# Kernel tuning notes

Measured on AMD Instinct MI355X. Metric: run time of the kernel, lower is better.

The kernel has to match this reference:

```python
import jax, jax.numpy as jnp
import numpy as np

N, E, IN_DIM, HID = 100000, 1600000, 128, 256
AA_DIM, POS_DIM, MAX_POS = 64, 32, 512


def setup_inputs() -> dict:
    key = jax.random.key(0)
    ks = jax.random.split(key, 16)
    x = jax.random.normal(ks[0], (N, IN_DIM), dtype=jnp.float32)
    edge_index = jax.random.randint(ks[1], (2, E), 0, N, dtype=jnp.int64)
    edge_weight = jax.random.uniform(ks[2], (E,), dtype=jnp.float32)
    mut_mask = jnp.zeros((N,), dtype=jnp.float32).at[123].set(1.0)  # one-hot mutation site
    wt_idx = jax.random.randint(ks[3], (1,), 0, 20, dtype=jnp.int64)
    mut_idx = jax.random.randint(ks[4], (1,), 0, 20, dtype=jnp.int64)
    def glorot(k, shape):
        fan = shape[0] + shape[1]
        return jax.random.uniform(k, shape, jnp.float32, -1.0, 1.0) * np.sqrt(6.0 / fan)
    W1 = glorot(ks[5], (IN_DIM, HID)); b1 = jnp.zeros((HID,), jnp.float32)
    W2 = glorot(ks[6], (HID, HID));    b2 = jnp.zeros((HID,), jnp.float32)
    aa_emb = jax.random.normal(ks[7], (20, AA_DIM), dtype=jnp.float32)
    pos_emb = jax.random.normal(ks[8], (MAX_POS, POS_DIM), dtype=jnp.float32)
    FEAT = HID + AA_DIM * 3 + POS_DIM  # 480
    Wh1 = glorot(ks[9], (FEAT, 512));  bh1 = jnp.zeros((512,), jnp.float32)
    Wh2 = glorot(ks[10], (512, 128));  bh2 = jnp.zeros((128,), jnp.float32)
    Wh3 = glorot(ks[11], (128, 1));    bh3 = jnp.zeros((1,), jnp.float32)
    return dict(x=x, edge_index=edge_index, edge_weight=edge_weight, mut_mask=mut_mask,
                wt_idx=wt_idx, mut_idx=mut_idx, W1=W1, b1=b1, W2=W2, b2=b2,
                aa_emb=aa_emb, pos_emb=pos_emb, Wh1=Wh1, bh1=bh1, Wh2=Wh2, bh2=bh2,
                Wh3=Wh3, bh3=bh3)


def _gcn_conv(x, W, b, row, col, ew, n):
    # PyG GCNConv: h = x W; out[col] += norm * h[row]; norm = d^-1/2[row]*ew*d^-1/2[col]
    deg = jax.ops.segment_sum(ew, col, num_segments=n)
    dinv = jnp.where(deg > 0, jax.lax.rsqrt(jnp.maximum(deg, 1e-12)), 0.0)
    norm = dinv[row] * ew * dinv[col]
    h = x @ W
    out = jax.ops.segment_sum(h[row] * norm[:, None], col, num_segments=n)
    return out + b


def reference(x, edge_index, edge_weight, mut_mask, wt_idx, mut_idx,
              W1, b1, W2, b2, aa_emb, pos_emb, Wh1, bh1, Wh2, bh2, Wh3, bh3):
    n = x.shape[0]
    # add self loops with weight 1 (GCNConv default, fill_value=1.0)
    loop = jnp.arange(n, dtype=edge_index.dtype)
    row = jnp.concatenate([edge_index[0], loop])
    col = jnp.concatenate([edge_index[1], loop])
    ew = jnp.concatenate([edge_weight, jnp.ones((n,), edge_weight.dtype)])
    # encode (dropout is identity in eval mode)
    h = jax.nn.relu(_gcn_conv(x, W1, b1, row, col, ew, n))
    h = jax.nn.relu(_gcn_conv(h, W2, b2, row, col, ew, n))
    # masked sum -> [1, HID]
    z = (h * mut_mask[:, None]).sum(axis=0, keepdims=True)
    wt = aa_emb[wt_idx.reshape(-1)]
    mut = aa_emb[mut_idx.reshape(-1)]
    delta = mut - wt
    pos = jnp.clip(jnp.argmax(mut_mask), 0, pos_emb.shape[0] - 1).reshape(1)
    pe = pos_emb[pos]
    feat = jnp.concatenate([z, wt, mut, delta, pe], axis=1)  # [1, 480]
    f = jax.nn.relu(feat @ Wh1 + bh1)
    f = jax.nn.relu(f @ Wh2 + bh2)
    out = f @ Wh3 + bh3  # [1, 1]
    return out[0, 0]
```

## Files before the change

### kernel.cpp

```cpp
#include <hip/hip_runtime.h>


#define SCAP   512
#define L1CAP  512
#define L2CAP  16384
#define HID    256
#define INDIM  128

struct WsPtrs {
  int* cnt;
  float* deg;
  int* slot;
  int* s1;
  int* l1r; float* l1w;
  int* l2r; int* l2s; float* l2w;
  float* h1; float* h2;
  int* wscol;
};

__global__ void kinit(WsPtrs w, const int* eiraw, const float* mask, int N, int E) {
  int g = blockIdx.x * blockDim.x + threadIdx.x;
  int gs = gridDim.x * blockDim.x;
  for (int j = g; j < N; j += gs) {
    w.slot[j] = -1;
    float m = mask[j];
    if (m > 0.f) w.cnt[4] = j;
  }
  for (int j = g; j < SCAP * HID; j += gs) w.h1[j] = 0.f;
  if (g < HID) w.h2[g] = 0.f;
  if (g < 3)   w.cnt[g] = 0;
  if (g == 3) {
    int is64 = 1;
    long step = E / 20; if (step < 1) step = 1;
    for (int j = 1; j <= 16; ++j) {
      long idx = (long)j * step; if (idx >= E) break;
      if (eiraw[2 * idx + 1] != 0) { is64 = 0; break; }
    }
    w.cnt[3] = is64;
  }
}

__device__ __forceinline__ void reg_s1(WsPtrs& w, int r) {
  int old = atomicCAS(&w.slot[r], -1, -2);
  if (old == -1) {
    w.deg[r] = 1.0f;
    int idx = atomicAdd(&w.cnt[1], 1);
    if (idx < SCAP) { w.s1[idx] = r; w.slot[r] = idx; }
    else            { w.slot[r] = -3; }
  }
}

__global__ void kpassA(WsPtrs w, const int* eiraw, const float* ew, int E) {
  const int tgt = w.cnt[4];
  const bool is64 = w.cnt[3] != 0;
  const long long* ell = (const long long*)eiraw;
  int g = blockIdx.x * blockDim.x + threadIdx.x;
  int gs = gridDim.x * blockDim.x;
  for (long e = g; e < E; e += gs) {
    int c = is64 ? (int)ell[(long)E + e] : eiraw[(long)E + e];
    w.wscol[e] = c;
    if (c == tgt) {
      int r = is64 ? (int)ell[e] : eiraw[e];
      int i1 = atomicAdd(&w.cnt[0], 1);
      if (i1 < L1CAP) { w.l1r[i1] = r; w.l1w[i1] = ew[e]; }
      reg_s1(w, r);
    }
  }
  if (g == 0) {
    int i1 = atomicAdd(&w.cnt[0], 1);
    if (i1 < L1CAP) { w.l1r[i1] = tgt; w.l1w[i1] = 1.0f; }
    reg_s1(w, tgt);
  }
}

__global__ void kpassB(WsPtrs w, const int* eiraw, const float* ew, int E) {
  const bool is64 = w.cnt[3] != 0;
  const long long* ell = (const long long*)eiraw;
  int g = blockIdx.x * blockDim.x + threadIdx.x;
  int gs = gridDim.x * blockDim.x;
  int ns = w.cnt[1]; if (ns > SCAP) ns = SCAP;
  for (int j = g; j < ns; j += gs) {
    int idx = atomicAdd(&w.cnt[2], 1);
    if (idx < L2CAP) { w.l2r[idx] = w.s1[j]; w.l2s[idx] = j; w.l2w[idx] = 1.0f; }
  }
  const int4* c4 = (const int4*)w.wscol;
  int nv = E >> 2;
  for (int j = g; j < nv; j += gs) {
    int4 v = c4[j];
    #pragma unroll
    for (int t = 0; t < 4; ++t) {
      int c = (t == 0) ? v.x : (t == 1) ? v.y : (t == 2) ? v.z : v.w;
      int s = w.slot[c];
      if (s >= 0) {
        long e = 4L * j + t;
        int r = is64 ? (int)ell[e] : eiraw[e];
        int idx = atomicAdd(&w.cnt[2], 1);
        if (idx < L2CAP) { w.l2r[idx] = r; w.l2s[idx] = s; w.l2w[idx] = ew[e]; }
        int old = atomicCAS(&w.slot[r], -1, -3);
        if (old == -1) w.deg[r] = 1.0f;
      }
    }
  }
  for (long e = 4L * nv + g; e < E; e += gs) {
    int c = w.wscol[e];
    int s = w.slot[c];
    if (s >= 0) {
      int r = is64 ? (int)ell[e] : eiraw[e];
      int idx = atomicAdd(&w.cnt[2], 1);
      if (idx < L2CAP) { w.l2r[idx] = r; w.l2s[idx] = s; w.l2w[idx] = ew[e]; }
      int old = atomicCAS(&w.slot[r], -1, -3);
      if (old == -1) w.deg[r] = 1.0f;
    }
  }
}

__global__ void kpassC(WsPtrs w, const float* ew, int E) {
  int g = blockIdx.x * blockDim.x + threadIdx.x;
  int gs = gridDim.x * blockDim.x;
  const int4* c4 = (const int4*)w.wscol;
  int nv = E >> 2;
  for (int j = g; j < nv; j += gs) {
    int4 v = c4[j];
    #pragma unroll
    for (int t = 0; t < 4; ++t) {
      int c = (t == 0) ? v.x : (t == 1) ? v.y : (t == 2) ? v.z : v.w;
      if (w.slot[c] != -1) atomicAdd(&w.deg[c], ew[4L * j + t]);
    }
  }
  for (long e = 4L * nv + g; e < E; e += gs) {
    int c = w.wscol[e];
    if (w.slot[c] != -1) atomicAdd(&w.deg[c], ew[e]);
  }
}

__global__ void kh1(WsPtrs w, const float* x, const float* W1) {
  __shared__ float xs[INDIM];
  int n = w.cnt[2]; if (n > L2CAP) n = L2CAP;
  int tid = threadIdx.x;
  for (int b = blockIdx.x; b < n; b += gridDim.x) {
    int r = w.l2r[b], s = w.l2s[b];
    float wt = w.l2w[b];
    int c = w.s1[s];
    float norm = rsqrtf(w.deg[r]) * wt * rsqrtf(w.deg[c]);
    if (tid < INDIM) xs[tid] = x[(long)r * INDIM + tid];
    __syncthreads();
    float acc = 0.f;
    #pragma unroll 8
    for (int k = 0; k < INDIM; ++k) acc += xs[k] * W1[k * HID + tid];
    atomicAdd(&w.h1[s * HID + tid], norm * acc);
    __syncthreads();
  }
}

__global__ void kh2(WsPtrs w, const float* W2, const float* b1) {
  __shared__ float hs[HID];
  int n = w.cnt[0]; if (n > L1CAP) n = L1CAP;
  int tid = threadIdx.x;
  int tgt = w.cnt[4];
  float dti = rsqrtf(w.deg[tgt]);
  for (int b = blockIdx.x; b < n; b += gridDim.x) {
    int v = w.l1r[b]; float wt = w.l1w[b];
    int s = w.slot[v];
    hs[tid] = (s >= 0) ? fmaxf(w.h1[s * HID + tid] + b1[tid], 0.f) : 0.f;
    __syncthreads();
    float norm = rsqrtf(w.deg[v]) * wt * dti;
    float acc = 0.f;
    #pragma unroll 8
    for (int k = 0; k < HID; ++k) acc += hs[k] * W2[k * HID + tid];
    atomicAdd(&w.h2[tid], norm * acc);
    __syncthreads();
  }
}

__global__ void __launch_bounds__(1024) khead(
    WsPtrs w, const float* b2, const float* mask,
    const int* wtI_, const int* mutI_,
    const float* aa, const float* pemb,
    const float* Wh1, const float* bh1,
    const float* Wh2, const float* bh2,
    const float* Wh3, const float* bh3,
    float* out) {
  __shared__ float feat[480];
  __shared__ float f1[512];
  __shared__ float pp[1024];
  __shared__ float f2[128];
  int t = threadIdx.x;
  int tgt = w.cnt[4];
  if (t < HID) feat[t] = fmaxf(w.h2[t] + b2[t], 0.f) * mask[tgt];
  int wtI = wtI_[0], mutI = mutI_[0];
  if (t < 64) {
    float a = aa[wtI * 64 + t];
    float b = aa[mutI * 64 + t];
    feat[256 + t] = a; feat[320 + t] = b; feat[384 + t] = b - a;
  }
  int pos = tgt; if (pos > 511) pos = 511; if (pos < 0) pos = 0;
  if (t < 32) feat[448 + t] = pemb[pos * 32 + t];
  __syncthreads();
  {
    int o = t & 511, half = t >> 9;
    int k0 = half * 240, k1 = k0 + 240;
    float v = 0.f;
    for (int k = k0; k < k1; ++k) v += feat[k] * Wh1[k * 512 + o];
    pp[t] = v;
  }
  __syncthreads();
  if (t < 512) f1[t] = fmaxf(pp[t] + pp[t + 512] + bh1[t], 0.f);
  __syncthreads();
  {
    int o = t & 127, part = t >> 7;
    int k0 = part * 64, k1 = k0 + 64;
    float v = 0.f;
    for (int k = k0; k < k1; ++k) v += f1[k] * Wh2[k * 128 + o];
    pp[t] = v;
  }
  __syncthreads();
  if (t < 128) {
    float v = bh2[t];
    #pragma unroll
    for (int j = 0; j < 8; ++j) v += pp[j * 128 + t];
    f2[t] = fmaxf(v, 0.f) * Wh3[t];
  }
  __syncthreads();
  if (t == 0) {
    float s = bh3[0];
    for (int k = 0; k < 128; ++k) s += f2[k];
    out[0] = s;
  }
}

extern "C" void kernel_launch(void* const* d_in, const int* in_sizes, int n_in,
                              void* d_out, int out_size, void* d_ws, size_t ws_size,
                              hipStream_t stream) {
  const float* x    = (const float*)d_in[0];
  const int*   ei   = (const int*)d_in[1];
  const float* ew   = (const float*)d_in[2];
  const float* mask = (const float*)d_in[3];
  const int*   wtI  = (const int*)d_in[4];
  const int*   mutI = (const int*)d_in[5];
  const float* W1   = (const float*)d_in[6];
  const float* b1   = (const float*)d_in[7];
  const float* W2   = (const float*)d_in[8];
  const float* b2   = (const float*)d_in[9];
  const float* aa   = (const float*)d_in[10];
  const float* pemb = (const float*)d_in[11];
  const float* Wh1  = (const float*)d_in[12];
  const float* bh1  = (const float*)d_in[13];
  const float* Wh2  = (const float*)d_in[14];
  const float* bh2  = (const float*)d_in[15];
  const float* Wh3  = (const float*)d_in[16];
  const float* bh3  = (const float*)d_in[17];
  float* out = (float*)d_out;
  const int N = in_sizes[3];
  const int E = in_sizes[2];

  char* q = (char*)d_ws;
  auto take = [&](size_t bytes) -> char* {
    char* r = q; q += (bytes + 255) & ~(size_t)255; return r;
  };
  WsPtrs w;
  w.cnt   = (int*)take(64);
  w.deg   = (float*)take((size_t)N * 4);
  w.slot  = (int*)take((size_t)N * 4);
  w.s1    = (int*)take(SCAP * 4);
  w.l1r   = (int*)take(L1CAP * 4);
  w.l1w   = (float*)take(L1CAP * 4);
  w.l2r   = (int*)take(L2CAP * 4);
  w.l2s   = (int*)take(L2CAP * 4);
  w.l2w   = (float*)take(L2CAP * 4);
  w.h1    = (float*)take((size_t)SCAP * HID * 4);
  w.h2    = (float*)take(HID * 4);
  w.wscol = (int*)take((size_t)E * 4);

  kinit  <<<512, 256, 0, stream>>>(w, ei, mask, N, E);
  kpassA <<<2048, 256, 0, stream>>>(w, ei, ew, E);
  kpassB <<<1024, 256, 0, stream>>>(w, ei, ew, E);
  kpassC <<<1024, 256, 0, stream>>>(w, ew, E);
  kh1    <<<512, 256, 0, stream>>>(w, x, W1);
  kh2    <<<64, 256, 0, stream>>>(w, W2, b1);
  khead  <<<1, 1024, 0, stream>>>(w, b2, mask, wtI, mutI, aa, pemb,
                                  Wh1, bh1, Wh2, bh2, Wh3, bh3, out);
}
```

Baseline: 183.4 us.

## Aggregate inputs before W1 and fuse layer/head kernels with last-block reduction

Layer-1 aggregation now sums the normalized neighbour input rows for each 1-hop node first and applies W1 once per node, instead of doing one matmul per 2-hop edge. The slot table, the materialized column array and the separate degree pass are removed. Degrees are computed for all nodes inside the first edge pass. kh1, kh2 and khead are merged into one 64-block kernel that uses a last-block-done atomic counter to run W2 and the MLP head. The trade-offs are a degree atomic for every edge, a linear scan over the 1-hop list in shared memory for every edge in pass B, and serial per-neighbour row accumulation with single-block tail work.

```diff
diff --git a/kernel.cpp b/kernel.cpp
--- a/kernel.cpp
+++ b/kernel.cpp
@@ -4,49 +4,39 @@
 #define SCAP   512
 #define L1CAP  512
 #define L2CAP  16384
+#define MCAP   2048
 #define HID    256
 #define INDIM  128
+#define G4     64
 
 struct WsPtrs {
   int* cnt;
   float* deg;
-  int* slot;
   int* s1;
   int* l1r; float* l1w;
   int* l2r; int* l2s; float* l2w;
-  float* h1; float* h2;
-  int* wscol;
+  float* h2;
 };
 
 __global__ void kinit(WsPtrs w, const int* eiraw, const float* mask, int N, int E) {
   int g = blockIdx.x * blockDim.x + threadIdx.x;
   int gs = gridDim.x * blockDim.x;
   for (int j = g; j < N; j += gs) {
-    w.slot[j] = -1;
-    float m = mask[j];
-    if (m > 0.f) w.cnt[4] = j;
-  }
-  for (int j = g; j < SCAP * HID; j += gs) w.h1[j] = 0.f;
+    w.deg[j] = 1.0f;
+    if (mask[j] > 0.f) w.cnt[4] = j;
+  }
   if (g < HID) w.h2[g] = 0.f;
-  if (g < 3)   w.cnt[g] = 0;
+  if (g < 3) w.cnt[g] = 0;
+  if (g == 5) w.cnt[5] = 0;
   if (g == 3) {
-    int is64 = 1;
+    int bad = 0;
     long step = E / 20; if (step < 1) step = 1;
+    #pragma unroll
     for (int j = 1; j <= 16; ++j) {
-      long idx = (long)j * step; if (idx >= E) break;
-      if (eiraw[2 * idx + 1] != 0) { is64 = 0; break; }
-    }
-    w.cnt[3] = is64;
-  }
-}
-
-__device__ __forceinline__ void reg_s1(WsPtrs& w, int r) {
-  int old = atomicCAS(&w.slot[r], -1, -2);
-  if (old == -1) {
-    w.deg[r] = 1.0f;
-    int idx = atomicAdd(&w.cnt[1], 1);
-    if (idx < SCAP) { w.s1[idx] = r; w.slot[r] = idx; }
-    else            { w.slot[r] = -3; }
+      long idx = (long)j * step;
+      if (idx < E) bad |= (eiraw[2 * idx + 1] != 0);
+    }
+    w.cnt[3] = bad ? 0 : 1;
   }
 }
 
@@ -58,173 +48,172 @@
   int gs = gridDim.x * blockDim.x;
   for (long e = g; e < E; e += gs) {
     int c = is64 ? (int)ell[(long)E + e] : eiraw[(long)E + e];
-    w.wscol[e] = c;
+    float wt = ew[e];
+    atomicAdd(&w.deg[c], wt);
     if (c == tgt) {
       int r = is64 ? (int)ell[e] : eiraw[e];
       int i1 = atomicAdd(&w.cnt[0], 1);
-      if (i1 < L1CAP) { w.l1r[i1] = r; w.l1w[i1] = ew[e]; }
-      reg_s1(w, r);
+      if (i1 < L1CAP) { w.l1r[i1] = r; w.l1w[i1] = wt; }
     }
   }
   if (g == 0) {
     int i1 = atomicAdd(&w.cnt[0], 1);
     if (i1 < L1CAP) { w.l1r[i1] = tgt; w.l1w[i1] = 1.0f; }
-    reg_s1(w, tgt);
   }
 }
 
 __global__ void kpassB(WsPtrs w, const int* eiraw, const float* ew, int E) {
+  __shared__ int l1s[L1CAP];
+  __shared__ int s1s[SCAP];
+  __shared__ int nss;
   const bool is64 = w.cnt[3] != 0;
   const long long* ell = (const long long*)eiraw;
+  int n1 = w.cnt[0]; if (n1 > L1CAP) n1 = L1CAP;
+  for (int i = threadIdx.x; i < n1; i += blockDim.x) l1s[i] = w.l1r[i];
+  __syncthreads();
+  if (threadIdx.x == 0) {
+    int ns = 0;
+    for (int i = 0; i < n1; ++i) {
+      int v = l1s[i]; bool seen = false;
+      for (int j = 0; j < ns; ++j) if (s1s[j] == v) { seen = true; break; }
+      if (!seen && ns < SCAP) s1s[ns++] = v;
+    }
+    nss = ns;
+  }
+  __syncthreads();
+  int ns = nss;
+  if (blockIdx.x == 0) {
+    for (int j = threadIdx.x; j < ns; j += blockDim.x) w.s1[j] = s1s[j];
+    if (threadIdx.x == 0) w.cnt[1] = ns;
+  }
   int g = blockIdx.x * blockDim.x + threadIdx.x;
   int gs = gridDim.x * blockDim.x;
-  int ns = w.cnt[1]; if (ns > SCAP) ns = SCAP;
-  for (int j = g; j < ns; j += gs) {
-    int idx = atomicAdd(&w.cnt[2], 1);
-    if (idx < L2CAP) { w.l2r[idx] = w.s1[j]; w.l2s[idx] = j; w.l2w[idx] = 1.0f; }
-  }
-  const int4* c4 = (const int4*)w.wscol;
-  int nv = E >> 2;
-  for (int j = g; j < nv; j += gs) {
-    int4 v = c4[j];
-    #pragma unroll
-    for (int t = 0; t < 4; ++t) {
-      int c = (t == 0) ? v.x : (t == 1) ? v.y : (t == 2) ? v.z : v.w;
-      int s = w.slot[c];
-      if (s >= 0) {
-        long e = 4L * j + t;
-        int r = is64 ? (int)ell[e] : eiraw[e];
-        int idx = atomicAdd(&w.cnt[2], 1);
-        if (idx < L2CAP) { w.l2r[idx] = r; w.l2s[idx] = s; w.l2w[idx] = ew[e]; }
-        int old = atomicCAS(&w.slot[r], -1, -3);
-        if (old == -1) w.deg[r] = 1.0f;
-      }
-    }
-  }
-  for (long e = 4L * nv + g; e < E; e += gs) {
-    int c = w.wscol[e];
-    int s = w.slot[c];
+  for (long e = g; e < E; e += gs) {
+    int c = is64 ? (int)ell[(long)E + e] : eiraw[(long)E + e];
+    int s = -1;
+    for (int j = 0; j < ns; ++j) if (s1s[j] == c) { s = j; break; }
     if (s >= 0) {
       int r = is64 ? (int)ell[e] : eiraw[e];
       int idx = atomicAdd(&w.cnt[2], 1);
       if (idx < L2CAP) { w.l2r[idx] = r; w.l2s[idx] = s; w.l2w[idx] = ew[e]; }
-      int old = atomicCAS(&w.slot[r], -1, -3);
-      if (old == -1) w.deg[r] = 1.0f;
-    }
-  }
-}
-
-__global__ void kpassC(WsPtrs w, const float* ew, int E) {
-  int g = blockIdx.x * blockDim.x + threadIdx.x;
-  int gs = gridDim.x * blockDim.x;
-  const int4* c4 = (const int4*)w.wscol;
-  int nv = E >> 2;
-  for (int j = g; j < nv; j += gs) {
-    int4 v = c4[j];
-    #pragma unroll
-    for (int t = 0; t < 4; ++t) {
-      int c = (t == 0) ? v.x : (t == 1) ? v.y : (t == 2) ? v.z : v.w;
-      if (w.slot[c] != -1) atomicAdd(&w.deg[c], ew[4L * j + t]);
-    }
-  }
-  for (long e = 4L * nv + g; e < E; e += gs) {
-    int c = w.wscol[e];
-    if (w.slot[c] != -1) atomicAdd(&w.deg[c], ew[e]);
-  }
-}
-
-__global__ void kh1(WsPtrs w, const float* x, const float* W1) {
-  __shared__ float xs[INDIM];
-  int n = w.cnt[2]; if (n > L2CAP) n = L2CAP;
-  int tid = threadIdx.x;
-  for (int b = blockIdx.x; b < n; b += gridDim.x) {
-    int r = w.l2r[b], s = w.l2s[b];
-    float wt = w.l2w[b];
-    int c = w.s1[s];
-    float norm = rsqrtf(w.deg[r]) * wt * rsqrtf(w.deg[c]);
-    if (tid < INDIM) xs[tid] = x[(long)r * INDIM + tid];
-    __syncthreads();
-    float acc = 0.f;
-    #pragma unroll 8
-    for (int k = 0; k < INDIM; ++k) acc += xs[k] * W1[k * HID + tid];
-    atomicAdd(&w.h1[s * HID + tid], norm * acc);
-    __syncthreads();
-  }
-}
-
-__global__ void kh2(WsPtrs w, const float* W2, const float* b1) {
-  __shared__ float hs[HID];
-  int n = w.cnt[0]; if (n > L1CAP) n = L1CAP;
-  int tid = threadIdx.x;
-  int tgt = w.cnt[4];
-  float dti = rsqrtf(w.deg[tgt]);
-  for (int b = blockIdx.x; b < n; b += gridDim.x) {
-    int v = w.l1r[b]; float wt = w.l1w[b];
-    int s = w.slot[v];
-    hs[tid] = (s >= 0) ? fmaxf(w.h1[s * HID + tid] + b1[tid], 0.f) : 0.f;
-    __syncthreads();
-    float norm = rsqrtf(w.deg[v]) * wt * dti;
-    float acc = 0.f;
-    #pragma unroll 8
-    for (int k = 0; k < HID; ++k) acc += hs[k] * W2[k * HID + tid];
-    atomicAdd(&w.h2[tid], norm * acc);
-    __syncthreads();
-  }
-}
-
-__global__ void __launch_bounds__(1024) khead(
-    WsPtrs w, const float* b2, const float* mask,
+    }
+  }
+}
+
+__global__ void __launch_bounds__(256) khfused(
+    WsPtrs w, const float* x, const float* W1, const float* b1,
+    const float* W2, const float* b2, const float* mask,
     const int* wtI_, const int* mutI_,
     const float* aa, const float* pemb,
     const float* Wh1, const float* bh1,
     const float* Wh2, const float* bh2,
     const float* Wh3, const float* bh3,
     float* out) {
+  __shared__ int   l1rS[L1CAP];
+  __shared__ float l1wS[L1CAP];
+  __shared__ int   mr[MCAP];
+  __shared__ float mn[MCAP];
+  __shared__ int   mcnt;
+  __shared__ float xsum[INDIM];
+  __shared__ float hsL[HID];
   __shared__ float feat[480];
   __shared__ float f1[512];
-  __shared__ float pp[1024];
-  __shared__ float f2[128];
-  int t = threadIdx.x;
+  __shared__ float pp[256];
+  __shared__ int   lastFlag;
+
+  int tid = threadIdx.x;
   int tgt = w.cnt[4];
-  if (t < HID) feat[t] = fmaxf(w.h2[t] + b2[t], 0.f) * mask[tgt];
+  int ns = w.cnt[1]; if (ns > SCAP) ns = SCAP;
+  int n1 = w.cnt[0]; if (n1 > L1CAP) n1 = L1CAP;
+  int n2 = w.cnt[2]; if (n2 > L2CAP) n2 = L2CAP;
+  float dti = rsqrtf(w.deg[tgt]);
+
+  if (blockIdx.x < ns) {
+    for (int i = tid; i < n1; i += 256) { l1rS[i] = w.l1r[i]; l1wS[i] = w.l1w[i]; }
+    for (int s = blockIdx.x; s < ns; s += gridDim.x) {
+      int v = w.s1[s];
+      float dv = w.deg[v];
+      float dvi = rsqrtf(dv);
+      if (tid == 0) mcnt = 0;
+      __syncthreads();
+      for (int i = tid; i < n2; i += 256) {
+        if (w.l2s[i] == s) {
+          int p = atomicAdd(&mcnt, 1);
+          if (p < MCAP) {
+            int r = w.l2r[i];
+            mr[p] = r;
+            mn[p] = rsqrtf(w.deg[r]) * w.l2w[i] * dvi;
+          }
+        }
+      }
+      __syncthreads();
+      int m = mcnt; if (m > MCAP) m = MCAP;
+      if (tid < INDIM) {
+        float xacc = x[(long)v * INDIM + tid] / dv;
+        for (int p = 0; p < m; ++p)
+          xacc += mn[p] * x[(long)mr[p] * INDIM + tid];
+        xsum[tid] = xacc;
+      }
+      __syncthreads();
+      float h = b1[tid];
+      #pragma unroll 8
+      for (int k = 0; k < INDIM; ++k) h += xsum[k] * W1[k * HID + tid];
+      h = fmaxf(h, 0.f);
+      float wsum = 0.f;
+      for (int i = 0; i < n1; ++i) if (l1rS[i] == v) wsum += l1wS[i];
+      float av = dvi * wsum * dti;
+      atomicAdd(&w.h2[tid], av * h);
+      __syncthreads();
+    }
+  }
+
+  __threadfence();
+  if (tid == 0) {
+    int t = __hip_atomic_fetch_add(&w.cnt[5], 1, __ATOMIC_ACQ_REL,
+                                   __HIP_MEMORY_SCOPE_AGENT);
+    lastFlag = (t == (int)gridDim.x - 1);
+  }
+  __syncthreads();
+  if (!lastFlag) return;
+
+  hsL[tid] = __hip_atomic_load(&w.h2[tid], __ATOMIC_RELAXED,
+                               __HIP_MEMORY_SCOPE_AGENT);
+  __syncthreads();
+  float y = b2[tid];
+  #pragma unroll 8
+  for (int k = 0; k < HID; ++k) y += hsL[k] * W2[k * HID + tid];
+  feat[tid] = fmaxf(y, 0.f) * mask[tgt];
   int wtI = wtI_[0], mutI = mutI_[0];
-  if (t < 64) {
-    float a = aa[wtI * 64 + t];
-    float b = aa[mutI * 64 + t];
-    feat[256 + t] = a; feat[320 + t] = b; feat[384 + t] = b - a;
+  if (tid < 64) {
+    float a = aa[wtI * 64 + tid];
+    float b = aa[mutI * 64 + tid];
+    feat[256 + tid] = a; feat[320 + tid] = b; feat[384 + tid] = b - a;
   }
   int pos = tgt; if (pos > 511) pos = 511; if (pos < 0) pos = 0;
-  if (t < 32) feat[448 + t] = pemb[pos * 32 + t];
+  if (tid < 32) feat[448 + tid] = pemb[pos * 32 + tid];
+  __syncthreads();
+  float v0 = bh1[tid], v1 = bh1[tid + 256];
+  for (int k = 0; k < 480; ++k) {
+    float f = feat[k];
+    v0 += f * Wh1[k * 512 + tid];
+    v1 += f * Wh1[k * 512 + tid + 256];
+  }
+  f1[tid] = fmaxf(v0, 0.f); f1[tid + 256] = fmaxf(v1, 0.f);
   __syncthreads();
   {
-    int o = t & 511, half = t >> 9;
-    int k0 = half * 240, k1 = k0 + 240;
-    float v = 0.f;
-    for (int k = k0; k < k1; ++k) v += feat[k] * Wh1[k * 512 + o];
-    pp[t] = v;
-  }
-  __syncthreads();
-  if (t < 512) f1[t] = fmaxf(pp[t] + pp[t + 512] + bh1[t], 0.f);
-  __syncthreads();
-  {
-    int o = t & 127, part = t >> 7;
-    int k0 = part * 64, k1 = k0 + 64;
-    float v = 0.f;
-    for (int k = k0; k < k1; ++k) v += f1[k] * Wh2[k * 128 + o];
-    pp[t] = v;
-  }
-  __syncthreads();
-  if (t < 128) {
-    float v = bh2[t];
-    #pragma unroll
-    for (int j = 0; j < 8; ++j) v += pp[j * 128 + t];
-    f2[t] = fmaxf(v, 0.f) * Wh3[t];
-  }
-  __syncthreads();
-  if (t == 0) {
-    float s = bh3[0];
-    for (int k = 0; k < 128; ++k) s += f2[k];
-    out[0] = s;
+    int o = tid & 127, half = tid >> 7;
+    float vv = 0.f;
+    int k0 = half * 256;
+    for (int k = k0; k < k0 + 256; ++k) vv += f1[k] * Wh2[k * 128 + o];
+    pp[tid] = vv;
+  }
+  __syncthreads();
+  if (tid < 128) pp[tid] = fmaxf(pp[tid] + pp[tid + 128] + bh2[tid], 0.f) * Wh3[tid];
+  __syncthreads();
+  if (tid == 0) {
+    float sacc = bh3[0];
+    for (int k = 0; k < 128; ++k) sacc += pp[k];
+    out[0] = sacc;
   }
 }
 
@@ -258,25 +247,19 @@
     char* r = q; q += (bytes + 255) & ~(size_t)255; return r;
   };
   WsPtrs w;
-  w.cnt   = (int*)take(64);
-  w.deg   = (float*)take((size_t)N * 4);
-  w.slot  = (int*)take((size_t)N * 4);
-  w.s1    = (int*)take(SCAP * 4);
-  w.l1r   = (int*)take(L1CAP * 4);
-  w.l1w   = (float*)take(L1CAP * 4);
-  w.l2r   = (int*)take(L2CAP * 4);
-  w.l2s   = (int*)take(L2CAP * 4);
-  w.l2w   = (float*)take(L2CAP * 4);
-  w.h1    = (float*)take((size_t)SCAP * HID * 4);
-  w.h2    = (float*)take(HID * 4);
-  w.wscol = (int*)take((size_t)E * 4);
-
-  kinit  <<<512, 256, 0, stream>>>(w, ei, mask, N, E);
-  kpassA <<<2048, 256, 0, stream>>>(w, ei, ew, E);
-  kpassB <<<1024, 256, 0, stream>>>(w, ei, ew, E);
-  kpassC <<<1024, 256, 0, stream>>>(w, ew, E);
-  kh1    <<<512, 256, 0, stream>>>(w, x, W1);
-  kh2    <<<64, 256, 0, stream>>>(w, W2, b1);
-  khead  <<<1, 1024, 0, stream>>>(w, b2, mask, wtI, mutI, aa, pemb,
-                                  Wh1, bh1, Wh2, bh2, Wh3, bh3, out);
-}
+  w.cnt = (int*)take(64);
+  w.deg = (float*)take((size_t)N * 4);
+  w.s1  = (int*)take(SCAP * 4);
+  w.l1r = (int*)take(L1CAP * 4);
+  w.l1w = (float*)take(L1CAP * 4);
+  w.l2r = (int*)take(L2CAP * 4);
+  w.l2s = (int*)take(L2CAP * 4);
+  w.l2w = (float*)take(L2CAP * 4);
+  w.h2  = (float*)take(HID * 4);
+
+  kinit   <<<512, 256, 0, stream>>>(w, ei, mask, N, E);
+  kpassA  <<<2048, 256, 0, stream>>>(w, ei, ew, E);
+  kpassB  <<<1024, 256, 0, stream>>>(w, ei, ew, E);
+  khfused <<<G4, 256, 0, stream>>>(w, x, W1, b1, W2, b2, mask, wtI, mutI,
+                                   aa, pemb, Wh1, bh1, Wh2, bh2, Wh3, bh3, out);
+}
```

New measurement: 333.8 us. 82.0% more time.
